# Optimization experiments

Hardware: AMD Instinct MI355X
Metric: run time of the kernel (lower is better)

The kernel has to match this reference:

```python
import jax, jax.numpy as jnp
import numpy as np

D_MODEL, D_K, D_V, N_HEADS = 1024, 64, 64, 16
B, S = 8, 1024
NEG = -1e9
LN_EPS = 1e-5


def setup_inputs() -> dict:
    key = jax.random.key(0)
    ks = jax.random.split(key, 10)
    scale = 1.0 / np.sqrt(D_MODEL)
    return {
        "Q_in": jax.random.normal(ks[0], (B, S, D_MODEL), jnp.float32),
        "K_in": jax.random.normal(ks[1], (B, S, D_MODEL), jnp.float32),
        "V_in": jax.random.normal(ks[2], (B, S, D_MODEL), jnp.float32),
        "mask": jax.random.randint(ks[3], (B, S, S), 0, 2).astype(bool),
        "W_Q": jax.random.normal(ks[4], (D_MODEL, N_HEADS * D_K), jnp.float32) * scale,
        "W_K": jax.random.normal(ks[5], (D_MODEL, N_HEADS * D_K), jnp.float32) * scale,
        "W_V": jax.random.normal(ks[6], (D_MODEL, N_HEADS * D_V), jnp.float32) * scale,
        "W_fc": jax.random.normal(ks[7], (N_HEADS * D_V, D_MODEL), jnp.float32) * scale,
        "ln_gamma": jnp.ones((D_MODEL,), jnp.float32),
        "ln_beta": jnp.zeros((D_MODEL,), jnp.float32),
    }


def reference(Q_in, K_in, V_in, mask, W_Q, W_K, W_V, W_fc, ln_gamma, ln_beta):
    b = Q_in.shape[0]
    # projections -> (B, H, S, d)
    Q = (Q_in @ W_Q).reshape(b, -1, N_HEADS, D_K).transpose(0, 2, 1, 3)
    K = (K_in @ W_K).reshape(b, -1, N_HEADS, D_K).transpose(0, 2, 1, 3)
    V = (V_in @ W_V).reshape(b, -1, N_HEADS, D_V).transpose(0, 2, 1, 3)
    # scores (B, H, Sq, Sk)
    scores = jnp.einsum("bhqd,bhkd->bhqk", Q, K) / np.sqrt(D_K)
    scores = jnp.where(mask[:, None, :, :], NEG, scores)
    attn = jax.nn.softmax(scores, axis=-1)
    context = jnp.einsum("bhqk,bhkd->bhqd", attn, V)
    context = context.transpose(0, 2, 1, 3).reshape(b, -1, N_HEADS * D_V)
    out = context @ W_fc + Q_in  # residual
    mu = jnp.mean(out, axis=-1, keepdims=True)
    var = jnp.var(out, axis=-1, keepdims=True)
    out = (out - mu) * jax.lax.rsqrt(var + LN_EPS) * ln_gamma + ln_beta
    return out, attn
```

## Files before the change

kernel.cpp:

```cpp
#include <hip/hip_runtime.h>
#include <stdint.h>

typedef unsigned short u16;
typedef float f32x4 __attribute__((ext_vector_type(4)));
typedef short s16x8 __attribute__((ext_vector_type(8)));
typedef short s16x4 __attribute__((ext_vector_type(4)));

constexpr int B  = 8;
constexpr int S  = 1024;
constexpr int DM = 1024;
constexpr int H  = 16;
constexpr int M  = B * S;
constexpr float NEGINF = -1e9f;

__device__ __forceinline__ u16 f2bf(float f) {
    union { float f; uint32_t u; } v; v.f = f;
    uint32_t u = v.u;
    uint32_t r = 0x7FFFu + ((u >> 16) & 1u);
    return (u16)((u + r) >> 16);
}
__device__ __forceinline__ float bf2f(u16 h) {
    union { uint32_t u; float f; } v; v.u = ((uint32_t)h) << 16; return v.f;
}

__device__ __forceinline__ void gload16(const u16* g, u16* l) {
    __builtin_amdgcn_global_load_lds(
        (const __attribute__((address_space(1))) unsigned int*)g,
        (__attribute__((address_space(3))) unsigned int*)l, 16, 0, 0);
}

__global__ void cvt_all(const float* __restrict__ q, const float* __restrict__ k,
                        const float* __restrict__ v,
                        u16* __restrict__ xq, u16* __restrict__ xk, u16* __restrict__ xv) {
    const float* in; u16* out;
    if (blockIdx.y == 0)      { in = q; out = xq; }
    else if (blockIdx.y == 1) { in = k; out = xk; }
    else                      { in = v; out = xv; }
    int i = (blockIdx.x * 256 + threadIdx.x) * 4;
    float4 val = *(const float4*)(in + i);
    ushort4 o;
    o.x = f2bf(val.x); o.y = f2bf(val.y); o.z = f2bf(val.z); o.w = f2bf(val.w);
    *(ushort4*)(out + i) = o;
}

__global__ void transpose_all(const float* __restrict__ w0, const float* __restrict__ w1,
                              const float* __restrict__ w2, const float* __restrict__ w3,
                              u16* __restrict__ o0, u16* __restrict__ o1,
                              u16* __restrict__ o2, u16* __restrict__ o3) {
    const float* W; u16* Wt;
    switch (blockIdx.z) {
        case 0:  W = w0; Wt = o0; break;
        case 1:  W = w1; Wt = o1; break;
        case 2:  W = w2; Wt = o2; break;
        default: W = w3; Wt = o3; break;
    }
    __shared__ float tile[32][33];
    int n0 = blockIdx.x * 32, k0 = blockIdx.y * 32;
    int tx = threadIdx.x & 31, ty = threadIdx.x >> 5;
#pragma unroll
    for (int r = 0; r < 4; ++r)
        tile[ty + r*8][tx] = W[(size_t)(k0 + ty + r*8) * DM + n0 + tx];
    __syncthreads();
#pragma unroll
    for (int r = 0; r < 4; ++r)
        Wt[(size_t)(n0 + ty + r*8) * DM + k0 + tx] = f2bf(tile[tx][ty + r*8]);
}

template<int EPI>
__global__ __launch_bounds__(256, 2)
void gemm_bt(const u16* __restrict__ A, const u16* __restrict__ Bt,
             void* __restrict__ Cv, const float* __restrict__ resid)
{
    __shared__ u16 As[128 * 32];
    __shared__ u16 Bs[128 * 32];
    const int m0 = blockIdx.x * 128;
    const int n0 = blockIdx.y * 128;
    const int t = threadIdx.x;
    const int lane = t & 63;
    const int wid = t >> 6;
    const int wm = (wid >> 1) * 64;
    const int wn = (wid & 1) * 64;
    const int lr = lane & 15;
    const int lg = lane >> 4;

    const u16* Ag = A  + (size_t)(m0 + (t >> 2)) * 1024 + (t & 3) * 8;
    const u16* Bg = Bt + (size_t)(n0 + (t >> 2)) * 1024 + (t & 3) * 8;
    u16* Al = As + t * 8;
    u16* Bl = Bs + t * 8;

    f32x4 acc[4][4] = {};

    for (int kt = 0; kt < 32; ++kt) {
        const int ko = kt * 32;
        __syncthreads();
        gload16(Ag + ko,            Al);
        gload16(Ag + 64*1024 + ko,  Al + 64*32);
        gload16(Bg + ko,            Bl);
        gload16(Bg + 64*1024 + ko,  Bl + 64*32);
        __syncthreads();
        s16x8 af[4], bfr[4];
#pragma unroll
        for (int m = 0; m < 4; ++m)
            af[m] = *(const s16x8*)(As + (wm + m*16 + lr) * 32 + lg * 8);
#pragma unroll
        for (int n = 0; n < 4; ++n)
            bfr[n] = *(const s16x8*)(Bs + (wn + n*16 + lr) * 32 + lg * 8);
#pragma unroll
        for (int m = 0; m < 4; ++m)
#pragma unroll
            for (int n = 0; n < 4; ++n)
                acc[m][n] = __builtin_amdgcn_mfma_f32_16x16x32_bf16(af[m], bfr[n], acc[m][n], 0, 0, 0);
    }

#pragma unroll
    for (int m = 0; m < 4; ++m) {
#pragma unroll
        for (int n = 0; n < 4; ++n) {
            const int rg0 = m0 + wm + m*16 + lg*4;
            const int cg  = n0 + wn + n*16 + lr;
            if constexpr (EPI == 0) {
                u16* C = (u16*)Cv;
#pragma unroll
                for (int r = 0; r < 4; ++r)
                    C[(size_t)(rg0 + r) * 1024 + cg] = f2bf(acc[m][n][r]);
            } else if constexpr (EPI == 1) {
                u16* C = (u16*)Cv;
                const int bb = rg0 >> 10;
                const int s0 = rg0 & 1023;
                const int hh = cg >> 6;
                const int dd = cg & 63;
                ushort4 pk;
                pk.x = f2bf(acc[m][n][0]); pk.y = f2bf(acc[m][n][1]);
                pk.z = f2bf(acc[m][n][2]); pk.w = f2bf(acc[m][n][3]);
                *(ushort4*)(C + (size_t)((bb*16 + hh)*64 + dd) * 1024 + s0) = pk;
            } else {
                float* C = (float*)Cv;
#pragma unroll
                for (int r = 0; r < 4; ++r) {
                    size_t idx = (size_t)(rg0 + r) * 1024 + cg;
                    C[idx] = acc[m][n][r] + resid[idx];
                }
            }
        }
    }
}

__global__ __launch_bounds__(256, 2)
void attn_fused(const u16* __restrict__ Qp, const u16* __restrict__ Kp,
                const void* __restrict__ maskp, const u16* __restrict__ Vt,
                float* __restrict__ attn, u16* __restrict__ ctx)
{
    const int i  = blockIdx.x;
    const int qt = (i >> 3) & 63;
    const int g  = ((i >> 9) << 3) | (i & 7);
    const int h  = g & 15;
    const int b  = g >> 4;
    const int q0 = qt * 16;

    const int t = threadIdx.x;
    const int lane = t & 63;
    const int w = t >> 6;
    const int lr = lane & 15;
    const int lg = lane >> 4;

    constexpr int PLD = 1032;
    __shared__ u16 Plds[16][PLD];
    __shared__ float redB[4][16];

    uint32_t orv = 0;
    const uint32_t* mw = (const uint32_t*)maskp;
#pragma unroll
    for (int ii = 0; ii < 64; ++ii) orv |= mw[ii];
    const bool mask_bytes = (orv > 1u);

    const u16* qb = Qp + (size_t)(b*S + q0 + lr) * DM + h*64 + lg*8;
    s16x8 qf0 = *(const s16x8*)(qb);
    s16x8 qf1 = *(const s16x8*)(qb + 32);

    const size_t mrow = (size_t)b * S * S + (size_t)(q0 + lr) * S;

    s16x4 paf[16];
    float hs = 0.f;
#pragma unroll
    for (int nk = 0; nk < 16; ++nk) {
        const u16* kb = Kp + (size_t)(b*S + w*256 + nk*16 + lr) * DM + h*64 + lg*8;
        s16x8 kf0 = *(const s16x8*)(kb);
        s16x8 kf1 = *(const s16x8*)(kb + 32);
        int m0, m1, m2, m3;
        {
            const size_t off = mrow + w*256 + nk*16 + lg*4;
            if (mask_bytes) {
                uchar4 mb = *(const uchar4*)((const uint8_t*)maskp + off);
                m0 = mb.x; m1 = mb.y; m2 = mb.z; m3 = mb.w;
            } else {
                int4 mi = *(const int4*)((const int*)maskp + off);
                m0 = mi.x; m1 = mi.y; m2 = mi.z; m3 = mi.w;
            }
        }
        f32x4 cc = {};
        cc = __builtin_amdgcn_mfma_f32_16x16x32_bf16(kf0, qf0, cc, 0, 0, 0);
        cc = __builtin_amdgcn_mfma_f32_16x16x32_bf16(kf1, qf1, cc, 0, 0, 0);
        cc[0] = __expf(m0 ? NEGINF : cc[0] * 0.125f);
        cc[1] = __expf(m1 ? NEGINF : cc[1] * 0.125f);
        cc[2] = __expf(m2 ? NEGINF : cc[2] * 0.125f);
        cc[3] = __expf(m3 ? NEGINF : cc[3] * 0.125f);
        hs += cc[0] + cc[1] + cc[2] + cc[3];
        s16x4 pa;
        pa[0] = (short)f2bf(cc[0]); pa[1] = (short)f2bf(cc[1]);
        pa[2] = (short)f2bf(cc[2]); pa[3] = (short)f2bf(cc[3]);
        paf[nk] = pa;
        *(s16x4*)&Plds[lr][w*256 + nk*16 + lg*4] = pa;
    }

    hs += __shfl_xor(hs, 16, 64);
    hs += __shfl_xor(hs, 32, 64);
    if (lane < 16) redB[w][lr] = hs;
    __syncthreads();

    const float tot = redB[0][lr] + redB[1][lr] + redB[2][lr] + redB[3][lr];
    const float inv  = tot > 0.f ? 1.0f / tot : 0.f;
    const float fill = tot > 0.f ? 0.f : (1.0f / 1024.0f);
    float invr[4];
#pragma unroll
    for (int r = 0; r < 4; ++r) {
        const int row = lg*4 + r;
        const float tr = redB[0][row] + redB[1][row] + redB[2][row] + redB[3][row];
        invr[r] = tr > 0.f ? 1.0f / tr : 0.f;
    }

    float* arow = attn + (size_t)(b*H + h) * S * S + (size_t)(q0 + lr) * S + w*256 + lg*4;
#pragma unroll
    for (int nk = 0; nk < 16; ++nk) {
        float4 st;
        st.x = fmaf(bf2f((u16)paf[nk][0]), inv, fill);
        st.y = fmaf(bf2f((u16)paf[nk][1]), inv, fill);
        st.z = fmaf(bf2f((u16)paf[nk][2]), inv, fill);
        st.w = fmaf(bf2f((u16)paf[nk][3]), inv, fill);
        *(float4*)(arow + nk*16) = st;
    }

    const u16* vrow = Vt + ((size_t)g*64 + w*16 + lr) * S;
    f32x4 pacc = {};
#pragma unroll
    for (int kt = 0; kt < 32; ++kt) {
        s16x8 af = *(const s16x8*)&Plds[lr][kt*32 + lg*8];
        s16x8 vf = *(const s16x8*)(vrow + kt*32 + lg*8);
        pacc = __builtin_amdgcn_mfma_f32_16x16x32_bf16(af, vf, pacc, 0, 0, 0);
    }
#pragma unroll
    for (int r = 0; r < 4; ++r)
        ctx[(size_t)(b*S + q0 + lg*4 + r) * DM + h*64 + w*16 + lr] = f2bf(pacc[r] * invr[r]);
}

__global__ __launch_bounds__(256)
void layernorm(const float* __restrict__ x, const float* __restrict__ gamma,
               const float* __restrict__ beta, float* __restrict__ out)
{
    const int row = blockIdx.x;
    const int t = threadIdx.x;
    const float* xr = x + (size_t)row * DM;
    float4 v = *(const float4*)(xr + t*4);
    float s  = v.x + v.y + v.z + v.w;
    float s2 = v.x*v.x + v.y*v.y + v.z*v.z + v.w*v.w;
#pragma unroll
    for (int d = 1; d < 64; d <<= 1) {
        s  += __shfl_xor(s,  d, 64);
        s2 += __shfl_xor(s2, d, 64);
    }
    __shared__ float ls[4], ls2[4];
    if ((t & 63) == 0) { ls[t >> 6] = s; ls2[t >> 6] = s2; }
    __syncthreads();
    s  = ls[0] + ls[1] + ls[2] + ls[3];
    s2 = ls2[0] + ls2[1] + ls2[2] + ls2[3];
    const float mu  = s * (1.0f / DM);
    const float var = s2 * (1.0f / DM) - mu * mu;
    const float rs  = rsqrtf(var + 1e-5f);
    float4 g  = *(const float4*)(gamma + t*4);
    float4 bb = *(const float4*)(beta  + t*4);
    float4 o;
    o.x = (v.x - mu) * rs * g.x + bb.x;
    o.y = (v.y - mu) * rs * g.y + bb.y;
    o.z = (v.z - mu) * rs * g.z + bb.z;
    o.w = (v.w - mu) * rs * g.w + bb.w;
    *(float4*)(out + (size_t)row * DM + t*4) = o;
}

extern "C" void kernel_launch(void* const* d_in, const int* in_sizes, int n_in,
                              void* d_out, int out_size, void* d_ws, size_t ws_size,
                              hipStream_t stream) {
    const float* Qin  = (const float*)d_in[0];
    const float* Kin  = (const float*)d_in[1];
    const float* Vin  = (const float*)d_in[2];
    const void*  mask = d_in[3];
    const float* Wq   = (const float*)d_in[4];
    const float* Wk   = (const float*)d_in[5];
    const float* Wv   = (const float*)d_in[6];
    const float* Wfc  = (const float*)d_in[7];
    const float* gam  = (const float*)d_in[8];
    const float* bet  = (const float*)d_in[9];

    float* out  = (float*)d_out;
    float* attn = (float*)d_out + (size_t)M * DM;

    char* ws = (char*)d_ws;
    constexpr size_t SZ_X = (size_t)M * DM * 2;
    constexpr size_t SZ_W = (size_t)DM * DM * 2;
    u16* Xq  = (u16*)(ws);
    u16* Xk  = (u16*)(ws + SZ_X);
    u16* Xv  = (u16*)(ws + 2*SZ_X);
    u16* WqT = (u16*)(ws + 3*SZ_X);
    u16* WkT = (u16*)(ws + 3*SZ_X + SZ_W);
    u16* WvT = (u16*)(ws + 3*SZ_X + 2*SZ_W);
    u16* WfT = (u16*)(ws + 3*SZ_X + 3*SZ_W);
    u16* Qp  = (u16*)(ws + 3*SZ_X + 4*SZ_W);
    u16* Kp  = (u16*)(ws + 4*SZ_X + 4*SZ_W);
    u16* Vt  = (u16*)(ws + 5*SZ_X + 4*SZ_W);
    float* preLN = (float*)(ws);
    u16*   Ctx   = (u16*)(ws + 2*SZ_X);

    dim3 blk(256);
    cvt_all<<<dim3(M * DM / 1024, 3), blk, 0, stream>>>(Qin, Kin, Vin, Xq, Xk, Xv);
    transpose_all<<<dim3(32, 32, 4), blk, 0, stream>>>(Wq, Wk, Wv, Wfc, WqT, WkT, WvT, WfT);

    gemm_bt<0><<<dim3(64, 8), blk, 0, stream>>>(Xq, WqT, Qp, nullptr);
    gemm_bt<0><<<dim3(64, 8), blk, 0, stream>>>(Xk, WkT, Kp, nullptr);
    gemm_bt<1><<<dim3(64, 8), blk, 0, stream>>>(Xv, WvT, Vt, nullptr);

    attn_fused<<<dim3(8192), blk, 0, stream>>>(Qp, Kp, mask, Vt, attn, Ctx);

    gemm_bt<2><<<dim3(64, 8), blk, 0, stream>>>(Ctx, WfT, preLN, Qin);
    layernorm<<<dim3(M), blk, 0, stream>>>(preLN, gam, bet, out);
}
```

Measured before the change: 536.4 us.

## Split fused attention into separate score and PV kernels

Splits the fused attention kernel in two. The first kernel computes the masked softmax and writes the fp32 attention matrix. The second kernel rereads that matrix from global memory, converts it to bf16 and multiplies it by V. This drops the 33KB LDS P buffer and the per-row normalization from the first kernel, which may raise occupancy. In exchange it adds a full reread of the 512MB attention matrix and an extra launch. The PV path now uses the already normalized fp32 probabilities rather than bf16 unnormalized values, so masked-row fill handling also changes slightly.

Measured after the change: 781.0 us. +45.6%, slower.

```diff
diff --git a/kernel.cpp b/kernel.cpp
--- a/kernel.cpp
+++ b/kernel.cpp
@@ -146,9 +146,8 @@
 }
 
 __global__ __launch_bounds__(256, 2)
-void attn_fused(const u16* __restrict__ Qp, const u16* __restrict__ Kp,
-                const void* __restrict__ maskp, const u16* __restrict__ Vt,
-                float* __restrict__ attn, u16* __restrict__ ctx)
+void attn_scores(const u16* __restrict__ Qp, const u16* __restrict__ Kp,
+                 const void* __restrict__ maskp, float* __restrict__ attn)
 {
     const int i  = blockIdx.x;
     const int qt = (i >> 3) & 63;
@@ -163,8 +162,6 @@
     const int lr = lane & 15;
     const int lg = lane >> 4;
 
-    constexpr int PLD = 1032;
-    __shared__ u16 Plds[16][PLD];
     __shared__ float redB[4][16];
 
     uint32_t orv = 0;
@@ -209,24 +206,15 @@
         pa[0] = (short)f2bf(cc[0]); pa[1] = (short)f2bf(cc[1]);
         pa[2] = (short)f2bf(cc[2]); pa[3] = (short)f2bf(cc[3]);
         paf[nk] = pa;
-        *(s16x4*)&Plds[lr][w*256 + nk*16 + lg*4] = pa;
     }
 
     hs += __shfl_xor(hs, 16, 64);
     hs += __shfl_xor(hs, 32, 64);
     if (lane < 16) redB[w][lr] = hs;
     __syncthreads();
-
     const float tot = redB[0][lr] + redB[1][lr] + redB[2][lr] + redB[3][lr];
     const float inv  = tot > 0.f ? 1.0f / tot : 0.f;
     const float fill = tot > 0.f ? 0.f : (1.0f / 1024.0f);
-    float invr[4];
-#pragma unroll
-    for (int r = 0; r < 4; ++r) {
-        const int row = lg*4 + r;
-        const float tr = redB[0][row] + redB[1][row] + redB[2][row] + redB[3][row];
-        invr[r] = tr > 0.f ? 1.0f / tr : 0.f;
-    }
 
     float* arow = attn + (size_t)(b*H + h) * S * S + (size_t)(q0 + lr) * S + w*256 + lg*4;
 #pragma unroll
@@ -238,18 +226,44 @@
         st.w = fmaf(bf2f((u16)paf[nk][3]), inv, fill);
         *(float4*)(arow + nk*16) = st;
     }
-
-    const u16* vrow = Vt + ((size_t)g*64 + w*16 + lr) * S;
+}
+
+__global__ __launch_bounds__(256, 2)
+void attn_pv(const float* __restrict__ attn, const u16* __restrict__ Vt,
+             u16* __restrict__ ctx)
+{
+    const int i  = blockIdx.x;
+    const int qt = (i >> 3) & 63;
+    const int g  = ((i >> 9) << 3) | (i & 7);
+    const int h  = g & 15;
+    const int b  = g >> 4;
+    const int q0 = qt * 16;
+
+    const int t = threadIdx.x;
+    const int lane = t & 63;
+    const int w = t >> 6;
+    const int lr = lane & 15;
+    const int lg = lane >> 4;
+
+    const float* arow = attn + (size_t)(b*H + h) * S * S + (size_t)(q0 + lr) * S + lg*8;
+    const u16*   vrow = Vt + ((size_t)g*64 + w*16 + lr) * S + lg*8;
+
     f32x4 pacc = {};
 #pragma unroll
     for (int kt = 0; kt < 32; ++kt) {
-        s16x8 af = *(const s16x8*)&Plds[lr][kt*32 + lg*8];
-        s16x8 vf = *(const s16x8*)(vrow + kt*32 + lg*8);
+        float4 p0 = *(const float4*)(arow + kt*32);
+        float4 p1 = *(const float4*)(arow + kt*32 + 4);
+        s16x8 af;
+        af[0] = (short)f2bf(p0.x); af[1] = (short)f2bf(p0.y);
+        af[2] = (short)f2bf(p0.z); af[3] = (short)f2bf(p0.w);
+        af[4] = (short)f2bf(p1.x); af[5] = (short)f2bf(p1.y);
+        af[6] = (short)f2bf(p1.z); af[7] = (short)f2bf(p1.w);
+        s16x8 vf = *(const s16x8*)(vrow + kt*32);
         pacc = __builtin_amdgcn_mfma_f32_16x16x32_bf16(af, vf, pacc, 0, 0, 0);
     }
 #pragma unroll
     for (int r = 0; r < 4; ++r)
-        ctx[(size_t)(b*S + q0 + lg*4 + r) * DM + h*64 + w*16 + lr] = f2bf(pacc[r] * invr[r]);
+        ctx[(size_t)(b*S + q0 + lg*4 + r) * DM + h*64 + w*16 + lr] = f2bf(pacc[r]);
 }
 
 __global__ __launch_bounds__(256)
@@ -326,7 +340,8 @@
     gemm_bt<0><<<dim3(64, 8), blk, 0, stream>>>(Xk, WkT, Kp, nullptr);
     gemm_bt<1><<<dim3(64, 8), blk, 0, stream>>>(Xv, WvT, Vt, nullptr);
 
-    attn_fused<<<dim3(8192), blk, 0, stream>>>(Qp, Kp, mask, Vt, attn, Ctx);
+    attn_scores<<<dim3(8192), blk, 0, stream>>>(Qp, Kp, mask, attn);
+    attn_pv<<<dim3(8192), blk, 0, stream>>>(attn, Vt, Ctx);
 
     gemm_bt<2><<<dim3(64, 8), blk, 0, stream>>>(Ctx, WfT, preLN, Qin);
     layernorm<<<dim3(M), blk, 0, stream>>>(preLN, gam, bet, out);
```

## Double-buffer K, mask and V global loads with explicit waitcnt pipelining in attention

Applied to the files above, without the earlier changes.

Replaces the plain QK and PV loops in the attention kernel with a two-stage software pipeline. K, mask and V tiles are loaded ahead through inline-asm global loads, and explicit s_waitcnt plus sched_barrier calls overlap memory latency with MFMA and exp work. This adds register pressure from the in-flight buffers. The hand-written vmcnt counts must match the number of loads issued: each QK stage issues 12 loads when the mask is int32 and also when it is bytes. Stores to the attention output are not counted in vmcnt on this path, but the inline asm bypasses the compiler's own wait tracking, which risks correctness.

Result: slower. 548.0 us (+2.2%).

```diff
diff --git a/kernel.cpp b/kernel.cpp
--- a/kernel.cpp
+++ b/kernel.cpp
@@ -5,6 +5,7 @@
 typedef float f32x4 __attribute__((ext_vector_type(4)));
 typedef short s16x8 __attribute__((ext_vector_type(8)));
 typedef short s16x4 __attribute__((ext_vector_type(4)));
+typedef int   i32x4 __attribute__((ext_vector_type(4)));
 
 constexpr int B  = 8;
 constexpr int S  = 1024;
@@ -179,38 +180,79 @@
 
     const size_t mrow = (size_t)b * S * S + (size_t)(q0 + lr) * S;
 
+    i32x4 kf0s[2][4], kf1s[2][4], mis[2][4];
+    int   mbs[2][4];
     s16x4 paf[16];
     float hs = 0.f;
-#pragma unroll
-    for (int nk = 0; nk < 16; ++nk) {
-        const u16* kb = Kp + (size_t)(b*S + w*256 + nk*16 + lr) * DM + h*64 + lg*8;
-        s16x8 kf0 = *(const s16x8*)(kb);
-        s16x8 kf1 = *(const s16x8*)(kb + 32);
-        int m0, m1, m2, m3;
-        {
-            const size_t off = mrow + w*256 + nk*16 + lg*4;
-            if (mask_bytes) {
-                uchar4 mb = *(const uchar4*)((const uint8_t*)maskp + off);
-                m0 = mb.x; m1 = mb.y; m2 = mb.z; m3 = mb.w;
-            } else {
-                int4 mi = *(const int4*)((const int*)maskp + off);
-                m0 = mi.x; m1 = mi.y; m2 = mi.z; m3 = mi.w;
-            }
-        }
-        f32x4 cc = {};
-        cc = __builtin_amdgcn_mfma_f32_16x16x32_bf16(kf0, qf0, cc, 0, 0, 0);
-        cc = __builtin_amdgcn_mfma_f32_16x16x32_bf16(kf1, qf1, cc, 0, 0, 0);
-        cc[0] = __expf(m0 ? NEGINF : cc[0] * 0.125f);
-        cc[1] = __expf(m1 ? NEGINF : cc[1] * 0.125f);
-        cc[2] = __expf(m2 ? NEGINF : cc[2] * 0.125f);
-        cc[3] = __expf(m3 ? NEGINF : cc[3] * 0.125f);
-        hs += cc[0] + cc[1] + cc[2] + cc[3];
-        s16x4 pa;
-        pa[0] = (short)f2bf(cc[0]); pa[1] = (short)f2bf(cc[1]);
-        pa[2] = (short)f2bf(cc[2]); pa[3] = (short)f2bf(cc[3]);
-        paf[nk] = pa;
-        *(s16x4*)&Plds[lr][w*256 + nk*16 + lg*4] = pa;
-    }
+
+#define QK_ISSUE(st, nb_) do {                                                      \
+    _Pragma("unroll")                                                               \
+    for (int j = 0; j < 4; ++j) {                                                   \
+        const u16* kb_ = Kp + (size_t)(b*S + w*256 + (nb_)*64 + j*16 + lr) * DM     \
+                            + h*64 + lg*8;                                          \
+        asm volatile("global_load_dwordx4 %0, %2, off\n\t"                          \
+                     "global_load_dwordx4 %1, %2, off offset:64"                    \
+                     : "=v"(kf0s[st][j]), "=v"(kf1s[st][j]) : "v"(kb_));            \
+        const size_t off_ = mrow + w*256 + (nb_)*64 + j*16 + lg*4;                  \
+        if (mask_bytes) {                                                           \
+            asm volatile("global_load_dword %0, %1, off"                            \
+                         : "=v"(mbs[st][j]) : "v"((const uint8_t*)maskp + off_));   \
+        } else {                                                                    \
+            asm volatile("global_load_dwordx4 %0, %1, off"                          \
+                         : "=v"(mis[st][j]) : "v"((const int*)maskp + off_));       \
+        }                                                                           \
+    }                                                                               \
+} while (0)
+
+#define QK_COMPUTE(st, nb_) do {                                                    \
+    _Pragma("unroll")                                                               \
+    for (int j = 0; j < 4; ++j) {                                                   \
+        const int nk_ = (nb_)*4 + j;                                                \
+        s16x8 kf0 = *(const s16x8*)&kf0s[st][j];                                    \
+        s16x8 kf1 = *(const s16x8*)&kf1s[st][j];                                    \
+        int m0_, m1_, m2_, m3_;                                                     \
+        if (mask_bytes) {                                                           \
+            int mm = mbs[st][j];                                                    \
+            m0_ = mm & 255; m1_ = (mm >> 8) & 255;                                  \
+            m2_ = (mm >> 16) & 255; m3_ = ((unsigned)mm) >> 24;                     \
+        } else {                                                                    \
+            m0_ = mis[st][j][0]; m1_ = mis[st][j][1];                               \
+            m2_ = mis[st][j][2]; m3_ = mis[st][j][3];                               \
+        }                                                                           \
+        f32x4 cc = {};                                                              \
+        cc = __builtin_amdgcn_mfma_f32_16x16x32_bf16(kf0, qf0, cc, 0, 0, 0);        \
+        cc = __builtin_amdgcn_mfma_f32_16x16x32_bf16(kf1, qf1, cc, 0, 0, 0);        \
+        cc[0] = __expf(m0_ ? NEGINF : cc[0] * 0.125f);                              \
+        cc[1] = __expf(m1_ ? NEGINF : cc[1] * 0.125f);                              \
+        cc[2] = __expf(m2_ ? NEGINF : cc[2] * 0.125f);                              \
+        cc[3] = __expf(m3_ ? NEGINF : cc[3] * 0.125f);                              \
+        hs += cc[0] + cc[1] + cc[2] + cc[3];                                        \
+        s16x4 pa;                                                                   \
+        pa[0] = (short)f2bf(cc[0]); pa[1] = (short)f2bf(cc[1]);                     \
+        pa[2] = (short)f2bf(cc[2]); pa[3] = (short)f2bf(cc[3]);                     \
+        paf[nk_] = pa;                                                              \
+        *(s16x4*)&Plds[lr][w*256 + nk_*16 + lg*4] = pa;                             \
+    }                                                                               \
+} while (0)
+
+    QK_ISSUE(0, 0);
+    QK_ISSUE(1, 1);
+    asm volatile("s_waitcnt vmcnt(12)");
+    __builtin_amdgcn_sched_barrier(0);
+    QK_COMPUTE(0, 0);
+    QK_ISSUE(0, 2);
+    asm volatile("s_waitcnt vmcnt(12)");
+    __builtin_amdgcn_sched_barrier(0);
+    QK_COMPUTE(1, 1);
+    QK_ISSUE(1, 3);
+    asm volatile("s_waitcnt vmcnt(12)");
+    __builtin_amdgcn_sched_barrier(0);
+    QK_COMPUTE(0, 2);
+    asm volatile("s_waitcnt vmcnt(0)");
+    __builtin_amdgcn_sched_barrier(0);
+    QK_COMPUTE(1, 3);
+#undef QK_ISSUE
+#undef QK_COMPUTE
 
     hs += __shfl_xor(hs, 16, 64);
     hs += __shfl_xor(hs, 32, 64);
@@ -240,13 +282,45 @@
     }
 
     const u16* vrow = Vt + ((size_t)g*64 + w*16 + lr) * S;
+    i32x4 vfs[2][8];
     f32x4 pacc = {};
-#pragma unroll
-    for (int kt = 0; kt < 32; ++kt) {
-        s16x8 af = *(const s16x8*)&Plds[lr][kt*32 + lg*8];
-        s16x8 vf = *(const s16x8*)(vrow + kt*32 + lg*8);
-        pacc = __builtin_amdgcn_mfma_f32_16x16x32_bf16(af, vf, pacc, 0, 0, 0);
-    }
+
+#define PV_ISSUE(st, kb_) do {                                                      \
+    _Pragma("unroll")                                                               \
+    for (int j = 0; j < 8; ++j) {                                                   \
+        asm volatile("global_load_dwordx4 %0, %1, off"                              \
+                     : "=v"(vfs[st][j]) : "v"(vrow + (kb_)*256 + j*32 + lg*8));     \
+    }                                                                               \
+} while (0)
+
+#define PV_COMPUTE(st, kb_) do {                                                    \
+    _Pragma("unroll")                                                               \
+    for (int j = 0; j < 8; ++j) {                                                   \
+        s16x8 af = *(const s16x8*)&Plds[lr][((kb_)*8 + j)*32 + lg*8];               \
+        s16x8 vf = *(const s16x8*)&vfs[st][j];                                      \
+        pacc = __builtin_amdgcn_mfma_f32_16x16x32_bf16(af, vf, pacc, 0, 0, 0);      \
+    }                                                                               \
+} while (0)
+
+    PV_ISSUE(0, 0);
+    PV_ISSUE(1, 1);
+    asm volatile("s_waitcnt vmcnt(8)");
+    __builtin_amdgcn_sched_barrier(0);
+    PV_COMPUTE(0, 0);
+    PV_ISSUE(0, 2);
+    asm volatile("s_waitcnt vmcnt(8)");
+    __builtin_amdgcn_sched_barrier(0);
+    PV_COMPUTE(1, 1);
+    PV_ISSUE(1, 3);
+    asm volatile("s_waitcnt vmcnt(8)");
+    __builtin_amdgcn_sched_barrier(0);
+    PV_COMPUTE(0, 2);
+    asm volatile("s_waitcnt vmcnt(0)");
+    __builtin_amdgcn_sched_barrier(0);
+    PV_COMPUTE(1, 3);
+#undef PV_ISSUE
+#undef PV_COMPUTE
+
 #pragma unroll
     for (int r = 0; r < 4; ++r)
         ctx[(size_t)(b*S + q0 + lg*4 + r) * DM + h*64 + w*16 + lr] = f2bf(pacc[r] * invr[r]);
```
